# Kernel tuning notes

Hardware: AMD Instinct MI355X
Metric: run time of the kernel (lower is better)

Reference implementation:

```python
import jax, jax.numpy as jnp
import numpy as np

NX, NQ, NU, B = 256, 256, 128, 8192
EPS = 1e-3
ALPHA = 0.0
STD = 0.5


def setup_inputs() -> dict:
    key = jax.random.key(0)
    ks = jax.random.split(key, 10)
    f32 = jnp.float32
    return {
        "t": 0,  # unused by the dynamics
        "xi": jax.random.normal(ks[0], (B, NX), f32),
        "u": jax.random.normal(ks[1], (B, NU), f32),
        "Pstar": STD * jax.random.normal(ks[2], (NX, NX), f32),
        "Chi": STD * jax.random.normal(ks[3], (NX, NQ), f32),
        "Y1": STD * jax.random.normal(ks[4], (NX, NX), f32),
        "B2": STD * jax.random.normal(ks[5], (NX, NU), f32),
        "D12": STD * jax.random.normal(ks[6], (NQ, NU), f32),
        "X": STD * jax.random.normal(ks[7], (NX + NQ, NX + NQ), f32),
        "bx": STD * jax.random.normal(ks[8], (NX, 1), f32),
        "bv": STD * jax.random.normal(ks[9], (NQ, 1), f32),
    }


def _derived(Pstar, Chi, Y1, X):
    # updateParameters(): build the contractive REN matrices from free params.
    P = 0.5 * (Pstar @ Pstar.T) + EPS * jnp.eye(NX, dtype=Pstar.dtype)
    H = X @ X.T + EPS * jnp.eye(NX + NQ, dtype=X.dtype)
    H1 = H[:NX, :NX]
    H2 = H[:NX, NX:]
    H4 = H[NX:, NX:]
    Y = -0.5 * (H1 + ALPHA * P + Y1 - Y1.T)
    lam = 0.5 * jnp.diagonal(H4)                      # diag of Lambda, [nq]
    Pinv = jnp.linalg.inv(P)
    A = Pinv @ Y                                      # F.linear(inv(P), Y.T)
    D11 = -jnp.tril(H4, -1) / lam[:, None]            # strictly lower-triangular
    C1 = Chi.T / lam[:, None]                         # [nq, nx]
    B1 = Pinv @ (-H2 - Chi)                           # [nx, nq]
    return A, B1, C1, D11


def reference(t, xi, u, Pstar, Chi, Y1, B2, D12, X, bx, bv):
    A, B1, C1, D11 = _derived(Pstar, Chi, Y1, X)
    # per-row affine part of v, precomputed as one GEMM: [B, nq]
    base = xi @ C1.T + u @ D12.T + bv[:, 0][None, :]
    # triangular recurrence: w_i = act(base_i + D11[i, :i] @ w[:i])
    # (D11 row 0 is zero, so including it for i=0 matches the torch loop)
    def step(w, inp):
        b_i, d_i, i = inp
        v = b_i + w @ d_i                             # [B]
        return w.at[:, i].set(jnp.tanh(v)), None
    w0 = jnp.zeros_like(base)
    w, _ = jax.lax.scan(step, w0, (base.T, D11, jnp.arange(NQ)))
    xi_dot = xi @ A.T + w @ B1.T + u @ B2.T + bx[:, 0][None, :]
    return xi_dot
```

## Files before the change

kernel.cpp:

```cpp
#include <hip/hip_runtime.h>

#define NXc 256
#define NQc 256
#define NUc 128
#define Bc  8192
#define NHc 512
#define EPSc 0.001f

template<bool BT>
__device__ inline void gemm_seg(const float* __restrict__ A, int lda,
                                const float* __restrict__ Bm, int ldb,
                                int m0, int n0, int K,
                                float acc[4][4], float* As, float* Bs)
{
    const int tid = threadIdx.x;
    const int tx = tid & 15, ty = tid >> 4;
    const int ar  = tid >> 3;
    const int akc = tid & 7;
    for (int k0 = 0; k0 < K; k0 += 32) {
        __syncthreads();
        #pragma unroll
        for (int it = 0; it < 2; ++it) {
            const int r = ar + it * 32;
            const float4 a4 = *(const float4*)&A[(m0 + r) * lda + k0 + akc * 4];
            As[(akc * 4 + 0) * 68 + r] = a4.x;
            As[(akc * 4 + 1) * 68 + r] = a4.y;
            As[(akc * 4 + 2) * 68 + r] = a4.z;
            As[(akc * 4 + 3) * 68 + r] = a4.w;
        }
        if constexpr (BT) {
            #pragma unroll
            for (int it = 0; it < 2; ++it) {
                const int n = ar + it * 32;
                const float4 b4 = *(const float4*)&Bm[(n0 + n) * ldb + k0 + akc * 4];
                Bs[(akc * 4 + 0) * 68 + n] = b4.x;
                Bs[(akc * 4 + 1) * 68 + n] = b4.y;
                Bs[(akc * 4 + 2) * 68 + n] = b4.z;
                Bs[(akc * 4 + 3) * 68 + n] = b4.w;
            }
        } else {
            const int bn4 = tid & 15;
            const int bk  = tid >> 4;
            #pragma unroll
            for (int it = 0; it < 2; ++it) {
                const int kk = bk + it * 16;
                *(float4*)&Bs[kk * 68 + bn4 * 4] =
                    *(const float4*)&Bm[(k0 + kk) * ldb + n0 + bn4 * 4];
            }
        }
        __syncthreads();
        #pragma unroll
        for (int kk = 0; kk < 32; ++kk) {
            const float4 a4 = *(const float4*)&As[kk * 68 + ty * 4];
            const float4 b4 = *(const float4*)&Bs[kk * 68 + tx * 4];
            const float av[4] = {a4.x, a4.y, a4.z, a4.w};
            const float bw[4] = {b4.x, b4.y, b4.z, b4.w};
            #pragma unroll
            for (int i = 0; i < 4; ++i)
                #pragma unroll
                for (int j = 0; j < 4; ++j)
                    acc[i][j] = __builtin_fmaf(av[i], bw[j], acc[i][j]);
        }
    }
}

__global__ __launch_bounds__(256) void k_gemm_sym(const float* __restrict__ S,
                                                  float* __restrict__ C,
                                                  int n, float alpha)
{
    __shared__ __align__(16) float As[32 * 68];
    __shared__ __align__(16) float Bs[32 * 68];
    float acc[4][4] = {};
    const int m0 = blockIdx.y * 64, n0 = blockIdx.x * 64;
    gemm_seg<true>(S, n, S, n, m0, n0, n, acc, As, Bs);
    const int tx = threadIdx.x & 15, ty = threadIdx.x >> 4;
    #pragma unroll
    for (int i = 0; i < 4; ++i)
        #pragma unroll
        for (int j = 0; j < 4; ++j) {
            int r = m0 + ty * 4 + i, c = n0 + tx * 4 + j;
            float v = alpha * acc[i][j];
            if (r == c) v += EPSc;
            C[r * n + c] = v;
        }
}

__global__ void k_derive(const float* __restrict__ H, const float* __restrict__ Chi,
                         const float* __restrict__ Y1,
                         float* __restrict__ YM, float* __restrict__ D11,
                         float* __restrict__ linv)
{
    const int i = blockIdx.x;
    const int j = threadIdx.x;
    const float li = 2.0f / H[(256 + i) * 512 + 256 + i];
    YM[i * 512 + j] = -0.5f * (H[i * 512 + j] + Y1[i * 256 + j] - Y1[j * 256 + i]);
    YM[i * 512 + 256 + j] = -H[i * 512 + 256 + j] - Chi[i * 256 + j];
    D11[i * 256 + j] = (j < i) ? (-H[(256 + i) * 512 + 256 + j] * li) : 0.0f;
    if (j == 0) linv[i] = li;
}

__global__ __launch_bounds__(256) void k_base(const float* __restrict__ xi,
                                              const float* __restrict__ u,
                                              const float* __restrict__ Chi,
                                              const float* __restrict__ D12,
                                              const float* __restrict__ bv,
                                              const float* __restrict__ linv,
                                              float* __restrict__ basew)
{
    __shared__ __align__(16) float As[32 * 68];
    __shared__ __align__(16) float Bs[32 * 68];
    float acc[4][4] = {};
    const int m0 = blockIdx.y * 64, n0 = blockIdx.x * 64;
    gemm_seg<false>(xi, 256, Chi, 256, m0, n0, 256, acc, As, Bs);
    const int tx = threadIdx.x & 15, ty = threadIdx.x >> 4;
    #pragma unroll
    for (int j = 0; j < 4; ++j) {
        float lv = linv[n0 + tx * 4 + j];
        #pragma unroll
        for (int i = 0; i < 4; ++i) acc[i][j] *= lv;
    }
    gemm_seg<true>(u, 128, D12, 128, m0, n0, 128, acc, As, Bs);
    #pragma unroll
    for (int i = 0; i < 4; ++i)
        #pragma unroll
        for (int j = 0; j < 4; ++j) {
            int r = m0 + ty * 4 + i, c = n0 + tx * 4 + j;
            basew[r * 256 + c] = acc[i][j] + bv[c];
        }
}

__device__ void gj_body(float* __restrict__ M, float* __restrict__ prbuf_raw)
{
    float (*prbuf)[256] = (float (*)[256])prbuf_raw;
    const int tid = threadIdx.x;
    const int tx = tid & 31;
    const int ty = tid >> 5;
    float m[8][8];
    #pragma unroll
    for (int ii = 0; ii < 8; ++ii)
        #pragma unroll
        for (int jj = 0; jj < 8; ++jj)
            m[ii][jj] = M[(ty * 8 + ii) * 256 + tx + 32 * jj];

    if (ty == 0) {
        #pragma unroll
        for (int jj = 0; jj < 8; ++jj) prbuf[0][tx + 32 * jj] = m[0][jj];
    }
    __syncthreads();

    #pragma unroll
    for (int kj = 0; kj < 8; ++kj) {
        #pragma unroll 1
        for (int kt = 0; kt < 32; ++kt) {
            const int k = kj * 32 + kt;
            const float* pr = prbuf[k & 1];
            float* prn = prbuf[(k + 1) & 1];
            const float pinv = 1.0f / pr[k];
            const int srcLane = (tid & 32) | kt;
            float prv[8], pcv[8];
            #pragma unroll
            for (int jj = 0; jj < 8; ++jj) prv[jj] = pr[tx + 32 * jj];
            #pragma unroll
            for (int ii = 0; ii < 8; ++ii) pcv[ii] = __shfl(m[ii][kj], srcLane);
            const bool colown = (tx == kt);
            #pragma unroll
            for (int ii = 0; ii < 8; ++ii) {
                const float fi = pcv[ii] * pinv;
                #pragma unroll
                for (int jj = 0; jj < 8; ++jj)
                    m[ii][jj] = __builtin_fmaf(-fi, prv[jj], m[ii][jj]);
                if (colown) m[ii][kj] = -fi;
            }
            if (ty == (k >> 3)) {
                const int kl = k & 7;
                #pragma unroll
                for (int ii = 0; ii < 8; ++ii) if (ii == kl) {
                    #pragma unroll
                    for (int jj = 0; jj < 8; ++jj) m[ii][jj] = prv[jj] * pinv;
                    if (colown) m[ii][kj] = pinv;
                }
            }
            if (ty == ((k + 1) >> 3)) {
                const int kl1 = (k + 1) & 7;
                #pragma unroll
                for (int ii = 0; ii < 8; ++ii) if (ii == kl1) {
                    #pragma unroll
                    for (int jj = 0; jj < 8; ++jj) prn[tx + 32 * jj] = m[ii][jj];
                }
            }
            __syncthreads();
        }
    }

    #pragma unroll
    for (int ii = 0; ii < 8; ++ii)
        #pragma unroll
        for (int jj = 0; jj < 8; ++jj)
            M[(ty * 8 + ii) * 256 + tx + 32 * jj] = m[ii][jj];
}

#define WPAD 264
__device__ void scan_body(const float* __restrict__ d11,
                          float* __restrict__ basew, int blk,
                          float* __restrict__ wls, float* __restrict__ dblk)
{
    const int tid = threadIdx.x;
    const int row0 = blk * 32;
    for (int idx = tid; idx < 32 * 64; idx += 1024) {
        int r = idx >> 6, c4 = idx & 63;
        *(float4*)&wls[r * WPAD + c4 * 4] =
            *(const float4*)&basew[(row0 + r) * 256 + c4 * 4];
    }
    __syncthreads();

    const bool act = (tid < 256);
    const int lane = tid & 63;
    const int t = lane & 7;
    const int rg = lane >> 3;
    const int r = (tid >> 6) * 8 + rg;
    float* rowp = act ? &wls[r * WPAD] : &wls[0];
    const int sr = tid >> 3, sc4 = tid & 7;

    #pragma unroll 1
    for (int c = 0; c < 8; ++c) {
        const int i0 = 32 * c;
        float acc[4] = {0.f, 0.f, 0.f, 0.f};
        if (act) {
            const float4 dv4 = *(const float4*)&d11[(i0 + sr) * 256 + i0 + sc4 * 4];
            dblk[sr * 33 + sc4 * 4 + 0] = dv4.x;
            dblk[sr * 33 + sc4 * 4 + 1] = dv4.y;
            dblk[sr * 33 + sc4 * 4 + 2] = dv4.z;
            dblk[sr * 33 + sc4 * 4 + 3] = dv4.w;
            const float* d0 = d11 + (i0 + t) * 256;
            for (int j = 0; j < i0; j += 4) {
                const float4 w4 = *(const float4*)&rowp[j];
                #pragma unroll
                for (int u = 0; u < 4; ++u) {
                    const float4 dv = *(const float4*)&d0[u * 8 * 256 + j];
                    acc[u] = __builtin_fmaf(w4.x, dv.x, acc[u]);
                    acc[u] = __builtin_fmaf(w4.y, dv.y, acc[u]);
                    acc[u] = __builtin_fmaf(w4.z, dv.z, acc[u]);
                    acc[u] = __builtin_fmaf(w4.w, dv.w, acc[u]);
                }
            }
            #pragma unroll
            for (int u = 0; u < 4; ++u) acc[u] += rowp[i0 + 8 * u + t];
        }
        __syncthreads();
        if (act) {
            #pragma unroll
            for (int jj = 0; jj < 32; ++jj) {
                const int o = jj & 7, uo = jj >> 3;
                const float x = acc[uo];
                const float v = 1.0f - 2.0f / (__expf(2.0f * x) + 1.0f);
                const float wj = __shfl(v, o, 8);
                if (t == o) rowp[i0 + jj] = v;
                #pragma unroll
                for (int u = 0; u < 4; ++u) {
                    if (8 * u + t > jj)
                        acc[u] = __builtin_fmaf(wj, dblk[(8 * u + t) * 33 + jj], acc[u]);
                }
            }
        }
        __syncthreads();
    }

    for (int idx = tid; idx < 32 * 64; idx += 1024) {
        int rr = idx >> 6, c4 = idx & 63;
        *(float4*)&basew[(row0 + rr) * 256 + c4 * 4] =
            *(const float4*)&wls[rr * WPAD + c4 * 4];
    }
}

__global__ __launch_bounds__(1024) void k_fat(float* __restrict__ Pm,
                                              const float* __restrict__ d11,
                                              float* __restrict__ basew)
{
    __shared__ __align__(16) float shmem[32 * WPAD + 32 * 33];
    if (blockIdx.x == 0) {
        gj_body(Pm, shmem);
    } else {
        scan_body(d11, basew, blockIdx.x - 1, shmem, shmem + 32 * WPAD);
    }
}

__global__ __launch_bounds__(256) void k_ab(const float* __restrict__ Pinv,
                                            const float* __restrict__ YM,
                                            float* __restrict__ AB)
{
    __shared__ __align__(16) float As[32 * 68];
    __shared__ __align__(16) float Bs[32 * 68];
    float acc[4][4] = {};
    const int m0 = blockIdx.y * 64, n0 = blockIdx.x * 64;
    gemm_seg<false>(Pinv, 256, YM, 512, m0, n0, 256, acc, As, Bs);
    const int tx = threadIdx.x & 15, ty = threadIdx.x >> 4;
    #pragma unroll
    for (int i = 0; i < 4; ++i)
        #pragma unroll
        for (int j = 0; j < 4; ++j)
            AB[(m0 + ty * 4 + i) * 512 + n0 + tx * 4 + j] = acc[i][j];
}

__global__ __launch_bounds__(256) void k_final(const float* __restrict__ xi,
                                               const float* __restrict__ w,
                                               const float* __restrict__ u,
                                               const float* __restrict__ AB,
                                               const float* __restrict__ B2,
                                               const float* __restrict__ bx,
                                               float* __restrict__ out)
{
    __shared__ __align__(16) float As[32 * 68];
    __shared__ __align__(16) float Bs[32 * 68];
    float acc[4][4] = {};
    const int m0 = blockIdx.y * 64, n0 = blockIdx.x * 64;
    gemm_seg<true>(xi, 256, AB, 512, m0, n0, 256, acc, As, Bs);
    gemm_seg<true>(w, 256, AB + 256, 512, m0, n0, 256, acc, As, Bs);
    gemm_seg<true>(u, 128, B2, 128, m0, n0, 128, acc, As, Bs);
    const int tx = threadIdx.x & 15, ty = threadIdx.x >> 4;
    #pragma unroll
    for (int i = 0; i < 4; ++i)
        #pragma unroll
        for (int j = 0; j < 4; ++j) {
            int r = m0 + ty * 4 + i, c = n0 + tx * 4 + j;
            out[r * 256 + c] = acc[i][j] + bx[c];
        }
}

extern "C" void kernel_launch(void* const* d_in, const int* in_sizes, int n_in,
                              void* d_out, int out_size, void* d_ws, size_t ws_size,
                              hipStream_t stream)
{
    (void)in_sizes; (void)n_in; (void)out_size; (void)ws_size;
    const float* xi    = (const float*)d_in[1];
    const float* u     = (const float*)d_in[2];
    const float* Pstar = (const float*)d_in[3];
    const float* Chi   = (const float*)d_in[4];
    const float* Y1    = (const float*)d_in[5];
    const float* B2    = (const float*)d_in[6];
    const float* D12   = (const float*)d_in[7];
    const float* X     = (const float*)d_in[8];
    const float* bx    = (const float*)d_in[9];
    const float* bv    = (const float*)d_in[10];
    float* out = (float*)d_out;

    float* ws    = (float*)d_ws;
    float* H     = ws;
    float* YM    = H + 262144;
    float* D11   = YM + 131072;
    float* linv  = D11 + 65536;
    float* Pm    = linv + 256;
    float* AB    = Pm + 65536;
    float* basew = AB + 131072;

    k_gemm_sym<<<dim3(8, 8), 256, 0, stream>>>(X, H, 512, 1.0f);
    k_gemm_sym<<<dim3(4, 4), 256, 0, stream>>>(Pstar, Pm, 256, 0.5f);
    k_derive  <<<dim3(256), 256, 0, stream>>>(H, Chi, Y1, YM, D11, linv);
    k_base    <<<dim3(4, 128), 256, 0, stream>>>(xi, u, Chi, D12, bv, linv, basew);
    k_fat     <<<dim3(257), 1024, 0, stream>>>(Pm, D11, basew);
    k_ab      <<<dim3(8, 4), 256, 0, stream>>>(Pm, YM, AB);
    k_final   <<<dim3(4, 128), 256, 0, stream>>>(xi, basew, u, AB, B2, bx, out);
}
```

Before: 390.2 us.

## Block Gauss-Jordan inversion by 4-row panels and widen triangular scan to all threads

The Gauss-Jordan inversion now eliminates four pivots per step. It inverts a 4x4 pivot block locally and applies a rank-4 update, which cuts the number of block-wide barriers from 256 to 64 and raises arithmetic per sync. The triangular tanh recurrence scan now uses all 1024 threads, one thread per (row, column) within each 32-column chunk, instead of 256 threads each handling four columns. This adds parallelism to the scan, at the cost of more redundant global reads of D11 and more shuffle traffic. The blocked elimination does no pivoting within each 4x4 block, which matches the unpivoted original.

```diff
diff --git a/kernel.cpp b/kernel.cpp
--- a/kernel.cpp
+++ b/kernel.cpp
@@ -129,9 +129,10 @@
         }
 }
 
-__device__ void gj_body(float* __restrict__ M, float* __restrict__ prbuf_raw)
-{
-    float (*prbuf)[256] = (float (*)[256])prbuf_raw;
+__device__ void gj_body(float* __restrict__ M, float* __restrict__ lds)
+{
+    float* R  = lds;
+    float* Rp = lds + 4 * 260;
     const int tid = threadIdx.x;
     const int tx = tid & 31;
     const int ty = tid >> 5;
@@ -144,52 +145,114 @@
 
     if (ty == 0) {
         #pragma unroll
-        for (int jj = 0; jj < 8; ++jj) prbuf[0][tx + 32 * jj] = m[0][jj];
+        for (int p = 0; p < 4; ++p)
+            #pragma unroll
+            for (int jj = 0; jj < 8; ++jj)
+                R[p * 260 + tx + 32 * jj] = m[p][jj];
     }
     __syncthreads();
 
-    #pragma unroll
-    for (int kj = 0; kj < 8; ++kj) {
-        #pragma unroll 1
-        for (int kt = 0; kt < 32; ++kt) {
-            const int k = kj * 32 + kt;
-            const float* pr = prbuf[k & 1];
-            float* prn = prbuf[(k + 1) & 1];
-            const float pinv = 1.0f / pr[k];
-            const int srcLane = (tid & 32) | kt;
-            float prv[8], pcv[8];
-            #pragma unroll
-            for (int jj = 0; jj < 8; ++jj) prv[jj] = pr[tx + 32 * jj];
-            #pragma unroll
-            for (int ii = 0; ii < 8; ++ii) pcv[ii] = __shfl(m[ii][kj], srcLane);
-            const bool colown = (tx == kt);
-            #pragma unroll
-            for (int ii = 0; ii < 8; ++ii) {
-                const float fi = pcv[ii] * pinv;
-                #pragma unroll
-                for (int jj = 0; jj < 8; ++jj)
-                    m[ii][jj] = __builtin_fmaf(-fi, prv[jj], m[ii][jj]);
-                if (colown) m[ii][kj] = -fi;
-            }
-            if (ty == (k >> 3)) {
-                const int kl = k & 7;
-                #pragma unroll
-                for (int ii = 0; ii < 8; ++ii) if (ii == kl) {
+    #pragma unroll 1
+    for (int g = 0; g < 64; ++g) {
+        const int k0 = g * 4;
+        const int jb0 = k0 >> 5;
+        const int lt0 = k0 & 31;
+        float d[4][4];
+        #pragma unroll
+        for (int p = 0; p < 4; ++p)
+            #pragma unroll
+            for (int q = 0; q < 4; ++q)
+                d[p][q] = R[p * 260 + k0 + q];
+        #pragma unroll
+        for (int k = 0; k < 4; ++k) {
+            const float pinv = 1.0f / d[k][k];
+            #pragma unroll
+            for (int i = 0; i < 4; ++i) if (i != k) {
+                const float f = d[i][k] * pinv;
+                #pragma unroll
+                for (int j = 0; j < 4; ++j) if (j != k)
+                    d[i][j] = __builtin_fmaf(-f, d[k][j], d[i][j]);
+                d[i][k] = -f;
+            }
+            #pragma unroll
+            for (int j = 0; j < 4; ++j) if (j != k) d[k][j] *= pinv;
+            d[k][k] = pinv;
+        }
+        {
+            const int p = tid >> 8;
+            const int col = tid & 255;
+            float v = 0.f;
+            #pragma unroll
+            for (int pp = 0; pp < 4; ++pp) if (pp == p) {
+                #pragma unroll
+                for (int q = 0; q < 4; ++q)
+                    v = __builtin_fmaf(d[pp][q], R[q * 260 + col], v);
+            }
+            Rp[p * 260 + col] = v;
+        }
+        __syncthreads();
+        const bool panelOwner = (ty == (k0 >> 3));
+        const int pii = k0 & 7;
+        #pragma unroll
+        for (int ii = 0; ii < 8; ++ii) {
+            float mv = 0.f;
+            #pragma unroll
+            for (int jb = 0; jb < 8; ++jb) if (jb == jb0) mv = m[ii][jb];
+            float ci[4];
+            #pragma unroll
+            for (int p = 0; p < 4; ++p)
+                ci[p] = __shfl(mv, (tid & 32) | (lt0 + p));
+            float fi[4];
+            #pragma unroll
+            for (int p = 0; p < 4; ++p) {
+                float s = 0.f;
+                #pragma unroll
+                for (int q = 0; q < 4; ++q)
+                    s = __builtin_fmaf(ci[q], d[q][p], s);
+                fi[p] = s;
+            }
+            #pragma unroll
+            for (int jj = 0; jj < 8; ++jj) {
+                const int col = tx + 32 * jj;
+                float upd = m[ii][jj];
+                #pragma unroll
+                for (int p = 0; p < 4; ++p)
+                    upd = __builtin_fmaf(-ci[p], Rp[p * 260 + col], upd);
+                if (jj == jb0) {
                     #pragma unroll
-                    for (int jj = 0; jj < 8; ++jj) m[ii][jj] = prv[jj] * pinv;
-                    if (colown) m[ii][kj] = pinv;
+                    for (int p = 0; p < 4; ++p)
+                        if (tx == lt0 + p) upd = -fi[p];
                 }
-            }
-            if (ty == ((k + 1) >> 3)) {
-                const int kl1 = (k + 1) & 7;
-                #pragma unroll
-                for (int ii = 0; ii < 8; ++ii) if (ii == kl1) {
+                m[ii][jj] = upd;
+            }
+            if (panelOwner) {
+                #pragma unroll
+                for (int pp = 0; pp < 4; ++pp) if (ii == pii + pp) {
                     #pragma unroll
-                    for (int jj = 0; jj < 8; ++jj) prn[tx + 32 * jj] = m[ii][jj];
+                    for (int jj = 0; jj < 8; ++jj) {
+                        float nv = Rp[pp * 260 + tx + 32 * jj];
+                        if (jj == jb0) {
+                            #pragma unroll
+                            for (int p = 0; p < 4; ++p)
+                                if (tx == lt0 + p) nv = d[pp][p];
+                        }
+                        m[ii][jj] = nv;
+                    }
                 }
             }
-            __syncthreads();
-        }
+        }
+        const int k1 = k0 + 4;
+        if (k1 < 256 && ty == (k1 >> 3)) {
+            const int pii1 = k1 & 7;
+            #pragma unroll
+            for (int ii = 0; ii < 8; ++ii)
+                #pragma unroll
+                for (int pp = 0; pp < 4; ++pp) if (ii == pii1 + pp)
+                    #pragma unroll
+                    for (int jj = 0; jj < 8; ++jj)
+                        R[pp * 260 + tx + 32 * jj] = m[ii][jj];
+        }
+        __syncthreads();
     }
 
     #pragma unroll
@@ -213,54 +276,38 @@
     }
     __syncthreads();
 
-    const bool act = (tid < 256);
-    const int lane = tid & 63;
-    const int t = lane & 7;
-    const int rg = lane >> 3;
-    const int r = (tid >> 6) * 8 + rg;
-    float* rowp = act ? &wls[r * WPAD] : &wls[0];
+    const int r = tid >> 5;
+    const int t = tid & 31;
+    float* rowp = &wls[r * WPAD];
     const int sr = tid >> 3, sc4 = tid & 7;
 
     #pragma unroll 1
     for (int c = 0; c < 8; ++c) {
         const int i0 = 32 * c;
-        float acc[4] = {0.f, 0.f, 0.f, 0.f};
-        if (act) {
+        if (tid < 256) {
             const float4 dv4 = *(const float4*)&d11[(i0 + sr) * 256 + i0 + sc4 * 4];
             dblk[sr * 33 + sc4 * 4 + 0] = dv4.x;
             dblk[sr * 33 + sc4 * 4 + 1] = dv4.y;
             dblk[sr * 33 + sc4 * 4 + 2] = dv4.z;
             dblk[sr * 33 + sc4 * 4 + 3] = dv4.w;
-            const float* d0 = d11 + (i0 + t) * 256;
-            for (int j = 0; j < i0; j += 4) {
-                const float4 w4 = *(const float4*)&rowp[j];
-                #pragma unroll
-                for (int u = 0; u < 4; ++u) {
-                    const float4 dv = *(const float4*)&d0[u * 8 * 256 + j];
-                    acc[u] = __builtin_fmaf(w4.x, dv.x, acc[u]);
-                    acc[u] = __builtin_fmaf(w4.y, dv.y, acc[u]);
-                    acc[u] = __builtin_fmaf(w4.z, dv.z, acc[u]);
-                    acc[u] = __builtin_fmaf(w4.w, dv.w, acc[u]);
-                }
-            }
-            #pragma unroll
-            for (int u = 0; u < 4; ++u) acc[u] += rowp[i0 + 8 * u + t];
-        }
-        __syncthreads();
-        if (act) {
-            #pragma unroll
-            for (int jj = 0; jj < 32; ++jj) {
-                const int o = jj & 7, uo = jj >> 3;
-                const float x = acc[uo];
-                const float v = 1.0f - 2.0f / (__expf(2.0f * x) + 1.0f);
-                const float wj = __shfl(v, o, 8);
-                if (t == o) rowp[i0 + jj] = v;
-                #pragma unroll
-                for (int u = 0; u < 4; ++u) {
-                    if (8 * u + t > jj)
-                        acc[u] = __builtin_fmaf(wj, dblk[(8 * u + t) * 33 + jj], acc[u]);
-                }
-            }
+        }
+        float acc = rowp[i0 + t];
+        const float* d0 = d11 + (i0 + t) * 256;
+        for (int j = 0; j < i0; j += 4) {
+            const float4 w4 = *(const float4*)&rowp[j];
+            const float4 dv = *(const float4*)&d0[j];
+            acc = __builtin_fmaf(w4.x, dv.x, acc);
+            acc = __builtin_fmaf(w4.y, dv.y, acc);
+            acc = __builtin_fmaf(w4.z, dv.z, acc);
+            acc = __builtin_fmaf(w4.w, dv.w, acc);
+        }
+        __syncthreads();
+        #pragma unroll
+        for (int jj = 0; jj < 32; ++jj) {
+            const float v = 1.0f - 2.0f / (__expf(2.0f * acc) + 1.0f);
+            const float wj = __shfl(v, jj, 32);
+            if (t == jj) rowp[i0 + jj] = v;
+            if (t > jj) acc = __builtin_fmaf(wj, dblk[t * 33 + jj], acc);
         }
         __syncthreads();
     }
```

After: 463.3 us. +18.7%, slower.

## Replace Gauss-Jordan inverse with Cholesky plus triangular solves; widen scan parallelism

Applied to the files above, without the earlier changes.

Replaces the explicit 256x256 Gauss-Jordan inversion of P with a packed-triangular Cholesky factorization in shared memory, then solves P·[A B1] = YM with forward/back triangular substitution in a new 16-block kernel instead of an inverse-times-matrix GEMM. The scan blocks are reorganized so all 1024 threads process one row column each (32 rows x 32 lanes) rather than 256 threads with four accumulators. The intent is to cut the serial critical path of the single inversion block that runs alongside the scan, at the cost of a serial triangular solve kernel and much larger shared memory per fat block (packed triangle ~128KB), which lowers scan-block occupancy.

```diff
diff --git a/kernel.cpp b/kernel.cpp
--- a/kernel.cpp
+++ b/kernel.cpp
@@ -129,74 +129,80 @@
         }
 }
 
-__device__ void gj_body(float* __restrict__ M, float* __restrict__ prbuf_raw)
-{
-    float (*prbuf)[256] = (float (*)[256])prbuf_raw;
+__device__ void chol_body(float* __restrict__ M, float* __restrict__ lt)
+{
     const int tid = threadIdx.x;
-    const int tx = tid & 31;
-    const int ty = tid >> 5;
-    float m[8][8];
-    #pragma unroll
-    for (int ii = 0; ii < 8; ++ii)
-        #pragma unroll
-        for (int jj = 0; jj < 8; ++jj)
-            m[ii][jj] = M[(ty * 8 + ii) * 256 + tx + 32 * jj];
-
-    if (ty == 0) {
-        #pragma unroll
-        for (int jj = 0; jj < 8; ++jj) prbuf[0][tx + 32 * jj] = m[0][jj];
+    for (int idx = tid; idx < 32896; idx += 1024) {
+        int i = (int)((sqrtf(8.0f * (float)idx + 1.0f) - 1.0f) * 0.5f);
+        while ((i + 1) * (i + 2) / 2 <= idx) ++i;
+        while (i * (i + 1) / 2 > idx) --i;
+        const int j = idx - i * (i + 1) / 2;
+        lt[idx] = M[i * 256 + j];
     }
     __syncthreads();
 
-    #pragma unroll
-    for (int kj = 0; kj < 8; ++kj) {
-        #pragma unroll 1
-        for (int kt = 0; kt < 32; ++kt) {
-            const int k = kj * 32 + kt;
-            const float* pr = prbuf[k & 1];
-            float* prn = prbuf[(k + 1) & 1];
-            const float pinv = 1.0f / pr[k];
-            const int srcLane = (tid & 32) | kt;
-            float prv[8], pcv[8];
-            #pragma unroll
-            for (int jj = 0; jj < 8; ++jj) prv[jj] = pr[tx + 32 * jj];
-            #pragma unroll
-            for (int ii = 0; ii < 8; ++ii) pcv[ii] = __shfl(m[ii][kj], srcLane);
-            const bool colown = (tx == kt);
-            #pragma unroll
-            for (int ii = 0; ii < 8; ++ii) {
-                const float fi = pcv[ii] * pinv;
-                #pragma unroll
-                for (int jj = 0; jj < 8; ++jj)
-                    m[ii][jj] = __builtin_fmaf(-fi, prv[jj], m[ii][jj]);
-                if (colown) m[ii][kj] = -fi;
+    #pragma unroll 1
+    for (int g = 0; g < 64; ++g) {
+        const int k0 = 4 * g;
+        const int o0 = (k0    ) * (k0 + 1) / 2 + k0;
+        const int o1 = (k0 + 1) * (k0 + 2) / 2 + k0;
+        const int o2 = (k0 + 2) * (k0 + 3) / 2 + k0;
+        const int o3 = (k0 + 3) * (k0 + 4) / 2 + k0;
+        float d00 = lt[o0];
+        float d10 = lt[o1], d11v = lt[o1 + 1];
+        float d20 = lt[o2], d21 = lt[o2 + 1], d22 = lt[o2 + 2];
+        float d30 = lt[o3], d31 = lt[o3 + 1], d32 = lt[o3 + 2], d33 = lt[o3 + 3];
+        d00 = sqrtf(d00);                 const float i00 = 1.0f / d00;
+        d10 *= i00; d20 *= i00; d30 *= i00;
+        d11v = sqrtf(d11v - d10 * d10);   const float i11 = 1.0f / d11v;
+        d21 = (d21 - d20 * d10) * i11;
+        d31 = (d31 - d30 * d10) * i11;
+        d22 = sqrtf(d22 - d20 * d20 - d21 * d21); const float i22 = 1.0f / d22;
+        d32 = (d32 - d30 * d20 - d31 * d21) * i22;
+        d33 = sqrtf(d33 - d30 * d30 - d31 * d31 - d32 * d32);
+        const float i33 = 1.0f / d33;
+        for (int i = k0 + 4 + tid; i < 256; i += 1024) {
+            const int o = i * (i + 1) / 2 + k0;
+            float a0 = lt[o], a1 = lt[o + 1], a2 = lt[o + 2], a3 = lt[o + 3];
+            a0 *= i00;
+            a1 = (a1 - a0 * d10) * i11;
+            a2 = (a2 - a0 * d20 - a1 * d21) * i22;
+            a3 = (a3 - a0 * d30 - a1 * d31 - a2 * d32) * i33;
+            lt[o] = a0; lt[o + 1] = a1; lt[o + 2] = a2; lt[o + 3] = a3;
+        }
+        __syncthreads();
+        if (tid == 0) {
+            lt[o0] = d00;
+            lt[o1] = d10; lt[o1 + 1] = d11v;
+            lt[o2] = d20; lt[o2 + 1] = d21; lt[o2 + 2] = d22;
+            lt[o3] = d30; lt[o3 + 1] = d31; lt[o3 + 2] = d32; lt[o3 + 3] = d33;
+        }
+        for (int j = k0 + 4 + tid; j < 256; j += 1024) {
+            const int oj = j * (j + 1) / 2 + k0;
+            const float p0 = lt[oj], p1 = lt[oj + 1], p2 = lt[oj + 2], p3 = lt[oj + 3];
+            int oi = oj;
+            for (int i = j; i < 256; ++i) {
+                const float q0 = lt[oi], q1 = lt[oi + 1];
+                const float q2 = lt[oi + 2], q3 = lt[oi + 3];
+                float v = lt[oi - k0 + j];
+                v = __builtin_fmaf(-q0, p0, v);
+                v = __builtin_fmaf(-q1, p1, v);
+                v = __builtin_fmaf(-q2, p2, v);
+                v = __builtin_fmaf(-q3, p3, v);
+                lt[oi - k0 + j] = v;
+                oi += i + 1;
             }
-            if (ty == (k >> 3)) {
-                const int kl = k & 7;
-                #pragma unroll
-                for (int ii = 0; ii < 8; ++ii) if (ii == kl) {
-                    #pragma unroll
-                    for (int jj = 0; jj < 8; ++jj) m[ii][jj] = prv[jj] * pinv;
-                    if (colown) m[ii][kj] = pinv;
-                }
-            }
-            if (ty == ((k + 1) >> 3)) {
-                const int kl1 = (k + 1) & 7;
-                #pragma unroll
-                for (int ii = 0; ii < 8; ++ii) if (ii == kl1) {
-                    #pragma unroll
-                    for (int jj = 0; jj < 8; ++jj) prn[tx + 32 * jj] = m[ii][jj];
-                }
-            }
-            __syncthreads();
-        }
-    }
-
-    #pragma unroll
-    for (int ii = 0; ii < 8; ++ii)
-        #pragma unroll
-        for (int jj = 0; jj < 8; ++jj)
-            M[(ty * 8 + ii) * 256 + tx + 32 * jj] = m[ii][jj];
+        }
+        __syncthreads();
+    }
+
+    for (int idx = tid; idx < 32896; idx += 1024) {
+        int i = (int)((sqrtf(8.0f * (float)idx + 1.0f) - 1.0f) * 0.5f);
+        while ((i + 1) * (i + 2) / 2 <= idx) ++i;
+        while (i * (i + 1) / 2 > idx) --i;
+        const int j = idx - i * (i + 1) / 2;
+        M[i * 256 + j] = lt[idx];
+    }
 }
 
 #define WPAD 264
@@ -213,54 +219,38 @@
     }
     __syncthreads();
 
-    const bool act = (tid < 256);
-    const int lane = tid & 63;
-    const int t = lane & 7;
-    const int rg = lane >> 3;
-    const int r = (tid >> 6) * 8 + rg;
-    float* rowp = act ? &wls[r * WPAD] : &wls[0];
+    const int r = tid >> 5;
+    const int t = tid & 31;
+    float* rowp = &wls[r * WPAD];
     const int sr = tid >> 3, sc4 = tid & 7;
 
     #pragma unroll 1
     for (int c = 0; c < 8; ++c) {
         const int i0 = 32 * c;
-        float acc[4] = {0.f, 0.f, 0.f, 0.f};
-        if (act) {
+        if (tid < 256) {
             const float4 dv4 = *(const float4*)&d11[(i0 + sr) * 256 + i0 + sc4 * 4];
             dblk[sr * 33 + sc4 * 4 + 0] = dv4.x;
             dblk[sr * 33 + sc4 * 4 + 1] = dv4.y;
             dblk[sr * 33 + sc4 * 4 + 2] = dv4.z;
             dblk[sr * 33 + sc4 * 4 + 3] = dv4.w;
-            const float* d0 = d11 + (i0 + t) * 256;
-            for (int j = 0; j < i0; j += 4) {
-                const float4 w4 = *(const float4*)&rowp[j];
-                #pragma unroll
-                for (int u = 0; u < 4; ++u) {
-                    const float4 dv = *(const float4*)&d0[u * 8 * 256 + j];
-                    acc[u] = __builtin_fmaf(w4.x, dv.x, acc[u]);
-                    acc[u] = __builtin_fmaf(w4.y, dv.y, acc[u]);
-                    acc[u] = __builtin_fmaf(w4.z, dv.z, acc[u]);
-                    acc[u] = __builtin_fmaf(w4.w, dv.w, acc[u]);
-                }
-            }
-            #pragma unroll
-            for (int u = 0; u < 4; ++u) acc[u] += rowp[i0 + 8 * u + t];
-        }
-        __syncthreads();
-        if (act) {
-            #pragma unroll
-            for (int jj = 0; jj < 32; ++jj) {
-                const int o = jj & 7, uo = jj >> 3;
-                const float x = acc[uo];
-                const float v = 1.0f - 2.0f / (__expf(2.0f * x) + 1.0f);
-                const float wj = __shfl(v, o, 8);
-                if (t == o) rowp[i0 + jj] = v;
-                #pragma unroll
-                for (int u = 0; u < 4; ++u) {
-                    if (8 * u + t > jj)
-                        acc[u] = __builtin_fmaf(wj, dblk[(8 * u + t) * 33 + jj], acc[u]);
-                }
-            }
+        }
+        float acc = rowp[i0 + t];
+        const float* d0 = d11 + (i0 + t) * 256;
+        for (int j = 0; j < i0; j += 4) {
+            const float4 w4 = *(const float4*)&rowp[j];
+            const float4 dv = *(const float4*)&d0[j];
+            acc = __builtin_fmaf(w4.x, dv.x, acc);
+            acc = __builtin_fmaf(w4.y, dv.y, acc);
+            acc = __builtin_fmaf(w4.z, dv.z, acc);
+            acc = __builtin_fmaf(w4.w, dv.w, acc);
+        }
+        __syncthreads();
+        #pragma unroll
+        for (int jj = 0; jj < 32; ++jj) {
+            const float v = 1.0f - 2.0f / (__expf(2.0f * acc) + 1.0f);
+            const float wj = __shfl(v, jj, 32);
+            if (t == jj) rowp[i0 + jj] = v;
+            if (t > jj) acc = __builtin_fmaf(wj, dblk[t * 33 + jj], acc);
         }
         __syncthreads();
     }
@@ -276,29 +266,88 @@
                                               const float* __restrict__ d11,
                                               float* __restrict__ basew)
 {
-    __shared__ __align__(16) float shmem[32 * WPAD + 32 * 33];
+    __shared__ __align__(16) float shmem[32896];
     if (blockIdx.x == 0) {
-        gj_body(Pm, shmem);
+        chol_body(Pm, shmem);
     } else {
         scan_body(d11, basew, blockIdx.x - 1, shmem, shmem + 32 * WPAD);
     }
 }
 
-__global__ __launch_bounds__(256) void k_ab(const float* __restrict__ Pinv,
-                                            const float* __restrict__ YM,
-                                            float* __restrict__ AB)
-{
-    __shared__ __align__(16) float As[32 * 68];
-    __shared__ __align__(16) float Bs[32 * 68];
-    float acc[4][4] = {};
-    const int m0 = blockIdx.y * 64, n0 = blockIdx.x * 64;
-    gemm_seg<false>(Pinv, 256, YM, 512, m0, n0, 256, acc, As, Bs);
-    const int tx = threadIdx.x & 15, ty = threadIdx.x >> 4;
-    #pragma unroll
-    for (int i = 0; i < 4; ++i)
-        #pragma unroll
-        for (int j = 0; j < 4; ++j)
-            AB[(m0 + ty * 4 + i) * 512 + n0 + tx * 4 + j] = acc[i][j];
+__global__ __launch_bounds__(1024) void k_trs(const float* __restrict__ L,
+                                              const float* __restrict__ YM,
+                                              float* __restrict__ AB)
+{
+    __shared__ __align__(16) float pan[32 * WPAD];
+    __shared__ float dblk[32 * 33];
+    __shared__ float dinv[256];
+    const int tid = threadIdx.x;
+    const int col0 = blockIdx.x * 32;
+    const int c = tid >> 5;
+    const int t = tid & 31;
+    float* colp = &pan[c * WPAD];
+
+    for (int i = t; i < 256; i += 32)
+        colp[i] = YM[i * 512 + col0 + c];
+    if (tid < 256) dinv[tid] = 1.0f / L[tid * 256 + tid];
+    __syncthreads();
+
+    #pragma unroll 1
+    for (int cb = 0; cb < 8; ++cb) {
+        const int i0 = cb * 32;
+        {
+            const int rr = tid >> 5, qq = tid & 31;
+            dblk[rr * 33 + qq] = (qq <= rr) ? L[(i0 + rr) * 256 + i0 + qq] : 0.0f;
+        }
+        float acc = colp[i0 + t];
+        const float* lrow = L + (i0 + t) * 256;
+        for (int j = 0; j < i0; j += 4) {
+            const float4 z4 = *(const float4*)&colp[j];
+            acc = __builtin_fmaf(-lrow[j    ], z4.x, acc);
+            acc = __builtin_fmaf(-lrow[j + 1], z4.y, acc);
+            acc = __builtin_fmaf(-lrow[j + 2], z4.z, acc);
+            acc = __builtin_fmaf(-lrow[j + 3], z4.w, acc);
+        }
+        __syncthreads();
+        #pragma unroll
+        for (int jj = 0; jj < 32; ++jj) {
+            const float v = acc * dinv[i0 + jj];
+            const float wj = __shfl(v, jj, 32);
+            if (t == jj) colp[i0 + jj] = v;
+            if (t > jj) acc = __builtin_fmaf(-wj, dblk[t * 33 + jj], acc);
+        }
+        __syncthreads();
+    }
+
+    #pragma unroll 1
+    for (int cb = 7; cb >= 0; --cb) {
+        const int i0 = cb * 32;
+        {
+            const int rr = tid >> 5, qq = tid & 31;
+            dblk[rr * 33 + qq] = (qq <= rr) ? L[(i0 + rr) * 256 + i0 + qq] : 0.0f;
+        }
+        float acc = colp[i0 + t];
+        const int i = i0 + t;
+        for (int j = i0 + 32; j < 256; j += 4) {
+            const float4 x4 = *(const float4*)&colp[j];
+            acc = __builtin_fmaf(-L[(j    ) * 256 + i], x4.x, acc);
+            acc = __builtin_fmaf(-L[(j + 1) * 256 + i], x4.y, acc);
+            acc = __builtin_fmaf(-L[(j + 2) * 256 + i], x4.z, acc);
+            acc = __builtin_fmaf(-L[(j + 3) * 256 + i], x4.w, acc);
+        }
+        __syncthreads();
+        #pragma unroll
+        for (int jj = 31; jj >= 0; --jj) {
+            const float v = acc * dinv[i0 + jj];
+            const float wj = __shfl(v, jj, 32);
+            if (t == jj) colp[i0 + jj] = v;
+            if (t < jj) acc = __builtin_fmaf(-wj, dblk[jj * 33 + t], acc);
+        }
+        __syncthreads();
+    }
+
+    for (int i = t; i < 256; i += 32)
+        AB[i * 512 + col0 + c] = colp[i];
 }
 
 __global__ __launch_bounds__(256) void k_final(const float* __restrict__ xi,
@@ -357,6 +406,6 @@
     k_derive  <<<dim3(256), 256, 0, stream>>>(H, Chi, Y1, YM, D11, linv);
     k_base    <<<dim3(4, 128), 256, 0, stream>>>(xi, u, Chi, D12, bv, linv, basew);
     k_fat     <<<dim3(257), 1024, 0, stream>>>(Pm, D11, basew);
-    k_ab      <<<dim3(8, 4), 256, 0, stream>>>(Pm, YM, AB);
+    k_trs     <<<dim3(16), 1024, 0, stream>>>(Pm, YM, AB);
     k_final   <<<dim3(4, 128), 256, 0, stream>>>(xi, basew, u, AB, B2, bx, out);
 }
```

Measured after the change: 934.6 us. 139% more time.
